# Performance work log

Hardware: AMD Instinct MI355X
Metric: run time of the kernel (lower is better)

Reference implementation:

```python
import jax, jax.numpy as jnp
import numpy as np
from itertools import product

N = 65536
G = 128          # voxel grid side
K = 27           # 3^3 kernel offsets
C_IN, C_HID, C_OUT = 3, 256, 128
EPS = 1e-5


def _build_neighbors():
    rng = np.random.default_rng(0)
    keys = np.sort(rng.choice(G ** 3, size=N, replace=False))
    coords = np.stack(np.unravel_index(keys, (G, G, G)), axis=-1)  # [N,3]
    offs = np.array(list(product([-1, 0, 1], repeat=3)), dtype=np.int64)  # [27,3]
    nc = coords[:, None, :] + offs[None, :, :]                       # [N,27,3]
    inb = ((nc >= 0) & (nc < G)).all(-1)
    nk = nc[..., 0] * G * G + nc[..., 1] * G + nc[..., 2]
    pos = np.clip(np.searchsorted(keys, np.clip(nk, 0, G ** 3 - 1)), 0, N - 1)
    found = inb & (keys[pos] == nk)
    idx = np.where(found, pos, 0).astype(np.int32)
    return idx, found


def setup_inputs() -> dict:
    key = jax.random.key(0)
    ks = jax.random.split(key, 12)
    idx, mask = _build_neighbors()
    s_in = 1.0 / np.sqrt(K * C_IN)
    s_h = 1.0 / np.sqrt(K * C_HID)
    return {
        "feats": jax.random.normal(ks[0], (N, C_IN), jnp.float32),
        "w_in": jax.random.normal(ks[1], (K, C_IN, C_HID), jnp.float32) * s_in,
        "g_in": jnp.ones((C_HID,), jnp.float32),
        "b_in": jnp.zeros((C_HID,), jnp.float32),
        "w_res": jax.random.normal(ks[2], (4, 2, K, C_HID, C_HID), jnp.float32) * s_h,
        "g_res": jnp.ones((4, 2, C_HID), jnp.float32),
        "b_res": jnp.zeros((4, 2, C_HID), jnp.float32),
        "w_out": jax.random.normal(ks[3], (C_HID, C_OUT), jnp.float32) / np.sqrt(C_HID),
        "nbr_idx": jnp.asarray(idx),
        "nbr_mask": jnp.asarray(mask),
    }


def sparse_conv(feats, W, idx, mask):
    # feats [N,Cin], W [K,Cin,Cout], idx/mask [N,K] -> gather-GEMM-scatter per offset
    def step(acc, xs):
        w_k, i_k, m_k = xs  # [Cin,Cout], [N], [N]
        g = feats[i_k] * m_k[:, None]
        return acc + g @ w_k, None
    init = jnp.zeros((feats.shape[0], W.shape[-1]), feats.dtype)
    out, _ = jax.lax.scan(step, init, (W, idx.T, mask.T.astype(feats.dtype)))
    return out


def bn(x, g, b):
    mu = x.mean(0)
    var = x.var(0)
    return (x - mu) * jax.lax.rsqrt(var + EPS) * g + b


def reference(feats, w_in, g_in, b_in, w_res, g_res, b_res, w_out, nbr_idx, nbr_mask):
    h = jax.nn.relu(bn(sparse_conv(feats, w_in, nbr_idx, nbr_mask), g_in, b_in))
    for i in range(4):  # 4 MinkowskiResBlocks
        r = jax.nn.relu(bn(sparse_conv(h, w_res[i, 0], nbr_idx, nbr_mask), g_res[i, 0], b_res[i, 0]))
        r = bn(sparse_conv(r, w_res[i, 1], nbr_idx, nbr_mask), g_res[i, 1], b_res[i, 1])
        h = jax.nn.relu(r + h)
    return h @ w_out  # kernel_size=1 output conv == pointwise linear
```

## Files before the change

### kernel.cpp

```cpp
#include <hip/hip_runtime.h>
#include <hip/hip_bf16.h>


#define NPTS 65536
#define CHID 256
#define CAP  4096
#define LBLK 256
#define CBLK 2048

typedef __bf16 bf16x8 __attribute__((ext_vector_type(8)));
typedef float  f32x4  __attribute__((ext_vector_type(4)));
typedef unsigned short u16x8 __attribute__((ext_vector_type(8)));

__device__ __forceinline__ float bf2f(unsigned short u) {
    union { float f; unsigned v; } x; x.v = ((unsigned)u) << 16; return x.f;
}
__device__ __forceinline__ unsigned short f2bf(float f) {
    union { float f; unsigned v; } x; x.f = f;
    unsigned r = x.v + 0x7fffu + ((x.v >> 16) & 1u);
    return (unsigned short)(r >> 16);
}

__device__ __forceinline__ void gload16(const void* g, void* l) {
    __builtin_amdgcn_global_load_lds(
        (const __attribute__((address_space(1))) void*)g,
        (__attribute__((address_space(3))) void*)l, 16, 0, 0);
}

__device__ __forceinline__ bool mk(const void* mask, int mflag, size_t i) {
    if (mflag) return ((const unsigned char*)mask)[i] != 0;
    return ((const int*)mask)[i] != 0;
}

__global__ void detect_mask(const unsigned char* __restrict__ m, int* __restrict__ flag) {
    int t = blockIdx.x * 256 + threadIdx.x;
    int any = 0;
    for (int i = t; i < 262144; i += 64 * 256)
        if ((i & 3) && m[i]) any = 1;
    if (any) atomicOr(flag, 1);
}

__global__ void pack_w(const float* __restrict__ w, unsigned short* __restrict__ wp) {
    __shared__ float tile[64][65];
    int m   = blockIdx.x;
    int tci = (blockIdx.y >> 2) * 64;
    int tco = (blockIdx.y & 3) * 64;
    const float* src = w + (size_t)m * 65536;
    unsigned short* dst = wp + (size_t)m * 65536;
    int t = threadIdx.x, c = t & 63, rg = t >> 6;
    for (int r = rg; r < 64; r += 4)
        tile[r][c] = src[(size_t)(tci + r) * 256 + tco + c];
    __syncthreads();
    for (int r = rg; r < 64; r += 4)
        dst[(size_t)(tco + r) * 256 + tci + c] = f2bf(tile[c][r]);
}

__global__ void pack_wout(const float* __restrict__ w, unsigned short* __restrict__ wp) {
    __shared__ float tile[64][65];
    int tco = blockIdx.x * 64, tci = blockIdx.y * 64;
    int t = threadIdx.x, c = t & 63, rg = t >> 6;
    for (int r = rg; r < 64; r += 4)
        tile[r][c] = w[(size_t)(tci + r) * 128 + tco + c];
    __syncthreads();
    for (int r = rg; r < 64; r += 4)
        wp[(size_t)(tco + r) * 256 + tci + c] = f2bf(tile[c][r]);
}

__global__ void pack_win(const float* __restrict__ w, unsigned short* __restrict__ wp) {
    __shared__ float tile[64][65];
    int cot = blockIdx.x * 64, kkt = blockIdx.y * 64;
    int t = threadIdx.x, c = t & 63, rg = t >> 6;
    for (int r = rg; r < 64; r += 4) {
        int kk = kkt + r;
        tile[r][c] = (kk < 81) ? w[(size_t)kk * 256 + cot + c] : 0.f;
    }
    __syncthreads();
    for (int r = rg; r < 64; r += 4)
        wp[(size_t)(cot + r) * 128 + kkt + c] = f2bf(tile[c][r]);
}

__global__ void count_lists(const void* __restrict__ mask, const int* __restrict__ mflagp,
                            int* __restrict__ blkcnt ) {
    int mflag = *mflagp;
    int tid = threadIdx.x, lane = tid & 63;
    int n = blockIdx.x * 256 + tid;
    __shared__ int lc[26];
    if (tid < 26) lc[tid] = 0;
    __syncthreads();
    unsigned vb = 0;
    for (int k = 0; k < 27; ++k) {
        if (k == 13) continue;
        if (mk(mask, mflag, (size_t)n * 27 + k)) vb |= 1u << k;
    }
    for (int k26 = 0; k26 < 26; ++k26) {
        int k = (k26 < 13) ? k26 : k26 + 1;
        unsigned long long b = __ballot((vb >> k) & 1);
        if (lane == 0) atomicAdd(&lc[k26], __popcll(b));
    }
    __syncthreads();
    if (tid < 26) blkcnt[tid * LBLK + blockIdx.x] = lc[tid];
}

__global__ void scan_lists(const int* __restrict__ blkcnt, int* __restrict__ bases,
                           int* __restrict__ cnt) {
    int t = threadIdx.x;
    if (t < 26) {
        int s = 0;
        for (int b = 0; b < LBLK; ++b) {
            bases[t * LBLK + b] = s;
            s += blkcnt[t * LBLK + b];
        }
        cnt[t] = s;
    }
}

__global__ void fill_lists(const int* __restrict__ idx, const void* __restrict__ mask,
                           const int* __restrict__ mflagp, const int* __restrict__ bases,
                           int* __restrict__ srcL, int* __restrict__ nbrEnt,
                           unsigned char* __restrict__ nbrCnt) {
    int mflag = *mflagp;
    int tid = threadIdx.x, lane = tid & 63, wave = tid >> 6;
    int n = blockIdx.x * 256 + tid;
    __shared__ int wcnt[4][26];
    unsigned vb = 0;
    for (int k = 0; k < 27; ++k) {
        if (k == 13) continue;
        if (mk(mask, mflag, (size_t)n * 27 + k)) vb |= 1u << k;
    }
    for (int k26 = 0; k26 < 26; ++k26) {
        int k = (k26 < 13) ? k26 : k26 + 1;
        unsigned long long b = __ballot((vb >> k) & 1);
        if (lane == 0) wcnt[wave][k26] = __popcll(b);
    }
    __syncthreads();
    int j = 0;
    for (int k26 = 0; k26 < 26; ++k26) {
        int k = (k26 < 13) ? k26 : k26 + 1;
        bool v = (vb >> k) & 1;
        unsigned long long b = __ballot(v);
        if (v) {
            int p = bases[k26 * LBLK + blockIdx.x] + __popcll(b & ((1ull << lane) - 1ull));
            for (int w = 0; w < wave; ++w) p += wcnt[w][k26];
            if (p < CAP) {
                srcL[k26 * CAP + p] = idx[(size_t)n * 27 + k];
                nbrEnt[n * 32 + j] = k26 * CAP + p;
                ++j;
            }
        }
    }
    nbrCnt[n] = (unsigned char)j;
}

__global__ __launch_bounds__(256, 2)
void convin_gemm(const float* __restrict__ feats, const unsigned short* __restrict__ win,
                 const int* __restrict__ idx, const void* __restrict__ mask,
                 const int* __restrict__ mflagp, unsigned short* __restrict__ yb) {
    __shared__ __align__(16) char A[16384];
    __shared__ __align__(16) char B[32768];
    const int mflag = *mflagp;
    const int tid = threadIdx.x, lane = tid & 63, wave = tid >> 6;
    const int m0 = blockIdx.x * 64;

    for (int i = 0; i < 4; ++i)
        *(f32x4*)&A[tid * 64 + i * 16] = f32x4{0.f, 0.f, 0.f, 0.f};
    __syncthreads();

    {
        int row = tid & 63, g = tid >> 6;
        int n = m0 + row;
        int swz = (row & 7) << 4;
        for (int k = g; k < 27; k += 4) {
            if (mk(mask, mflag, (size_t)n * 27 + k)) {
                int j = idx[(size_t)n * 27 + k];
                float f0 = feats[j * 3 + 0], f1 = feats[j * 3 + 1], f2 = feats[j * 3 + 2];
                int b0 = 2 * (3 * k + 0), b1 = b0 + 2, b2 = b0 + 4;
                *(unsigned short*)&A[row * 256 + (b0 ^ swz)] = f2bf(f0);
                *(unsigned short*)&A[row * 256 + (b1 ^ swz)] = f2bf(f1);
                *(unsigned short*)&A[row * 256 + (b2 ^ swz)] = f2bf(f2);
            }
        }
    }

    const char* wb = (const char*)win;
    f32x4 acc[4][4] = {};

    for (int ks = 0; ks < 2; ++ks) {
        __syncthreads();
        for (int i = 0; i < 8; ++i) {
            int chunk = wave * 8 + i;
            int o = chunk * 1024 + lane * 16;
            int corow = o >> 7;
            int inner = (o & 127) ^ ((corow & 7) << 4);
            gload16(wb + (size_t)corow * 256 + ks * 128 + inner, B + o);
        }
        __syncthreads();
        const int cw = wave * 64;
        for (int kk = 0; kk < 64; kk += 32) {
            int kl = kk + 8 * (lane >> 4);
            bf16x8 af[4], bfr[4];
            for (int mi = 0; mi < 4; ++mi) {
                int row = 16 * mi + (lane & 15);
                af[mi] = *(const bf16x8*)(A + row * 256 + ((ks * 128 + 2 * kl) ^ ((row & 7) << 4)));
            }
            for (int ni = 0; ni < 4; ++ni) {
                int corow = cw + 16 * ni + (lane & 15);
                bfr[ni] = *(const bf16x8*)(B + corow * 128 + ((2 * kl) ^ ((corow & 7) << 4)));
            }
            for (int mi = 0; mi < 4; ++mi)
                for (int ni = 0; ni < 4; ++ni)
                    acc[mi][ni] = __builtin_amdgcn_mfma_f32_16x16x32_bf16(af[mi], bfr[ni], acc[mi][ni], 0, 0, 0);
        }
    }

    const int cw = wave * 64;
    const int rq = 4 * (lane >> 4);
    const int colo = lane & 15;
    for (int mi = 0; mi < 4; ++mi)
        for (int ni = 0; ni < 4; ++ni) {
            int col = cw + 16 * ni + colo;
            for (int r = 0; r < 4; ++r) {
                float v = acc[mi][ni][r];
                float o = __shfl_xor(v, 1);
                if ((lane & 1) == 0) {
                    unsigned pk = (unsigned)f2bf(v) | ((unsigned)f2bf(o) << 16);
                    int row = m0 + 16 * mi + rq + r;
                    *(unsigned*)&yb[(size_t)row * CHID + col] = pk;
                }
            }
        }
}

template<bool GATHER>
__global__ __launch_bounds__(512, 1)
void conv_gemm(const unsigned short* __restrict__ hin,
               const unsigned short* __restrict__ Wp,
               unsigned short* __restrict__ yb,
               const int* __restrict__ cnt,
               const int* __restrict__ srcL) {
    __shared__ __align__(16) char lds[131072];
    __shared__ int ids_src[256];
    const int tid  = threadIdx.x;
    const int lane = tid & 63;
    const int wave = tid >> 6;
    const int wm = wave >> 2;
    const int wn = wave & 3;

    int k27 = 13, m0 = 0, k26 = 0, tile = 0, c = 0;
    if (GATHER) {
        k26 = blockIdx.x;
        k27 = (k26 < 13) ? k26 : k26 + 1;
        tile = blockIdx.y;
        c = min(cnt[k26], CAP);
        if (tile * 256 >= c) return;
        if (tid < 256) {
            int g = tile * 256 + tid;
            ids_src[tid] = (g < c) ? srcL[k26 * CAP + g] : 0;
        }
        __syncthreads();
    } else {
        m0 = blockIdx.x * 256;
    }
    const char* hbase = (const char*)hin;
    const char* wbase = (const char*)(Wp + (size_t)k27 * (CHID * CHID));

    f32x4 acc[8][4] = {};

    auto STAGE = [&](int buf, int ks) {
        const int ci0 = ks * 64;
        char* dst = lds + buf * 65536;
        #pragma unroll
        for (int i = 0; i < 8; ++i) {
            int o = (wave * 8 + i) * 1024 + lane * 16;
            const char* src;
            if (o < 32768) {
                int row = o >> 7;
                int inner = (o & 127) ^ ((row & 7) << 4);
                int grow = GATHER ? ids_src[row] : (m0 + row);
                src = hbase + (size_t)grow * 512 + ci0 * 2 + inner;
            } else {
                int bo = o - 32768;
                int corow = bo >> 7;
                int inner = (bo & 127) ^ ((corow & 7) << 4);
                src = wbase + (size_t)corow * 512 + ci0 * 2 + inner;
            }
            gload16(src, dst + o);
        }
    };

    auto COMPUTE = [&](int buf) {
        const char* A = lds + buf * 65536;
        const char* B = A + 32768;
        #pragma unroll
        for (int kk = 0; kk < 64; kk += 32) {
            int kl = kk + 8 * (lane >> 4);
            bf16x8 af[8], bfr[4];
            #pragma unroll
            for (int mi = 0; mi < 8; ++mi) {
                int row = wm * 128 + 16 * mi + (lane & 15);
                af[mi] = *(const bf16x8*)(A + row * 128 + ((2 * kl) ^ ((row & 7) << 4)));
            }
            #pragma unroll
            for (int ni = 0; ni < 4; ++ni) {
                int corow = wn * 64 + 16 * ni + (lane & 15);
                bfr[ni] = *(const bf16x8*)(B + corow * 128 + ((2 * kl) ^ ((corow & 7) << 4)));
            }
            #pragma unroll
            for (int mi = 0; mi < 8; ++mi)
                #pragma unroll
                for (int ni = 0; ni < 4; ++ni)
                    acc[mi][ni] = __builtin_amdgcn_mfma_f32_16x16x32_bf16(af[mi], bfr[ni], acc[mi][ni], 0, 0, 0);
        }
    };

    STAGE(0, 0);
    __syncthreads();
    int cur = 0;
    #pragma unroll
    for (int ks = 0; ks < 4; ++ks) {
        if (ks < 3) STAGE(cur ^ 1, ks + 1);
        COMPUTE(cur);
        __syncthreads();
        cur ^= 1;
    }

    const int rq = 4 * (lane >> 4);
    const int colo = lane & 15;
    #pragma unroll
    for (int mi = 0; mi < 8; ++mi)
        #pragma unroll
        for (int ni = 0; ni < 4; ++ni) {
            int col = wn * 64 + 16 * ni + colo;
            #pragma unroll
            for (int r = 0; r < 4; ++r) {
                float v = acc[mi][ni][r];
                float o = __shfl_xor(v, 1);
                if ((lane & 1) == 0) {
                    unsigned pk = (unsigned)f2bf(v) | ((unsigned)f2bf(o) << 16);
                    int rl = wm * 128 + 16 * mi + rq + r;
                    if (!GATHER) {
                        *(unsigned*)&yb[(size_t)(m0 + rl) * CHID + col] = pk;
                    } else {
                        int g = tile * 256 + rl;
                        if (g < c)
                            *(unsigned*)&yb[((size_t)k26 * CAP + g) * CHID + col] = pk;
                    }
                }
            }
        }
}

__global__ __launch_bounds__(256)
void combine_stats(unsigned short* __restrict__ Yb,
                   const unsigned short* __restrict__ buf,
                   const int* __restrict__ nbrEnt,
                   const unsigned char* __restrict__ nbrCnt,
                   float* __restrict__ part) {
    __shared__ float ssum[8][256];
    __shared__ float ssq[8][256];
    const int tid = threadIdx.x;
    const int grp = tid >> 5;
    const int c0  = (tid & 31) * 8;
    float s[8] = {}, s2[8] = {};
    const int row0 = blockIdx.x * 32;
    for (int it = 0; it < 4; ++it) {
        int row = row0 + it * 8 + grp;
        size_t off = (size_t)row * CHID + c0;
        u16x8 y = *(const u16x8*)&Yb[off];
        float v[8];
        #pragma unroll
        for (int q = 0; q < 8; ++q) v[q] = bf2f(y[q]);
        int cnt = nbrCnt[row];
        for (int j = 0; j < cnt; ++j) {
            int e = nbrEnt[row * 32 + j];
            u16x8 b = *(const u16x8*)&buf[(size_t)e * CHID + c0];
            #pragma unroll
            for (int q = 0; q < 8; ++q) v[q] += bf2f(b[q]);
        }
        u16x8 o;
        #pragma unroll
        for (int q = 0; q < 8; ++q) {
            o[q] = f2bf(v[q]);
            s[q] += v[q];
            s2[q] += v[q] * v[q];
        }
        *(u16x8*)&Yb[off] = o;
    }
    #pragma unroll
    for (int q = 0; q < 8; ++q) {
        ssum[grp][c0 + q] = s[q];
        ssq[grp][c0 + q]  = s2[q];
    }
    __syncthreads();
    float ts = 0.f, tq = 0.f;
    #pragma unroll
    for (int g = 0; g < 8; ++g) { ts += ssum[g][tid]; tq += ssq[g][tid]; }
    part[(size_t)blockIdx.x * 512 + tid]       = ts;
    part[(size_t)blockIdx.x * 512 + 256 + tid] = tq;
}

__global__ __launch_bounds__(256)
void bn_stats_vec(const unsigned short* __restrict__ Yb, float* __restrict__ part) {
    __shared__ float ssum[8][256];
    __shared__ float ssq[8][256];
    const int tid = threadIdx.x;
    const int grp = tid >> 5;
    const int c0  = (tid & 31) * 8;
    float s[8] = {}, s2[8] = {};
    const int row0 = blockIdx.x * 32;
    for (int it = 0; it < 4; ++it) {
        int row = row0 + it * 8 + grp;
        u16x8 y = *(const u16x8*)&Yb[(size_t)row * CHID + c0];
        #pragma unroll
        for (int q = 0; q < 8; ++q) {
            float v = bf2f(y[q]);
            s[q] += v; s2[q] += v * v;
        }
    }
    #pragma unroll
    for (int q = 0; q < 8; ++q) {
        ssum[grp][c0 + q] = s[q];
        ssq[grp][c0 + q]  = s2[q];
    }
    __syncthreads();
    float ts = 0.f, tq = 0.f;
    #pragma unroll
    for (int g = 0; g < 8; ++g) { ts += ssum[g][tid]; tq += ssq[g][tid]; }
    part[(size_t)blockIdx.x * 512 + tid]       = ts;
    part[(size_t)blockIdx.x * 512 + 256 + tid] = tq;
}

__global__ void reduce_stats(const float* __restrict__ part, float* __restrict__ st) {
    int gt = blockIdx.x * 256 + threadIdx.x;
    int c = gt & 511;
    int chunk = gt >> 9;
    float s = 0.f;
    for (int i = 0; i < CBLK / 16; ++i)
        s += part[(size_t)(chunk * (CBLK / 16) + i) * 512 + c];
    unsafeAtomicAdd(&st[c], s);
}

__global__ __launch_bounds__(256)
void bn_apply(const unsigned short* __restrict__ yb, const float* __restrict__ st,
              const float* __restrict__ g, const float* __restrict__ b,
              const unsigned short* __restrict__ res, unsigned short* __restrict__ hout) {
    const int tid = threadIdx.x;
    const int grp = tid >> 5;
    const int c0  = (tid & 31) * 8;
    float sc[8], bi[8];
    #pragma unroll
    for (int q = 0; q < 8; ++q) {
        float mean = st[c0 + q] * (1.f / NPTS);
        float var  = st[256 + c0 + q] * (1.f / NPTS) - mean * mean;
        float rstd = rsqrtf(var + 1e-5f);
        sc[q] = rstd * g[c0 + q];
        bi[q] = b[c0 + q] - mean * sc[q];
    }
    const int row0 = blockIdx.x * 32;
    for (int it = 0; it < 4; ++it) {
        int row = row0 + it * 8 + grp;
        size_t off = (size_t)row * CHID + c0;
        u16x8 y = *(const u16x8*)&yb[off];
        u16x8 o;
        if (res) {
            u16x8 rr = *(const u16x8*)&res[off];
            #pragma unroll
            for (int q = 0; q < 8; ++q) {
                float v = bf2f(y[q]) * sc[q] + bi[q] + bf2f(rr[q]);
                o[q] = f2bf(fmaxf(v, 0.f));
            }
        } else {
            #pragma unroll
            for (int q = 0; q < 8; ++q) {
                float v = bf2f(y[q]) * sc[q] + bi[q];
                o[q] = f2bf(fmaxf(v, 0.f));
            }
        }
        *(u16x8*)&hout[off] = o;
    }
}

__global__ __launch_bounds__(256, 2)
void gemm_out(const unsigned short* __restrict__ hin, const unsigned short* __restrict__ wop,
              float* __restrict__ out) {
    __shared__ __align__(16) char lds[16384 + 16384];
    const int tid = threadIdx.x, lane = tid & 63, wave = tid >> 6;
    const int m0 = blockIdx.x * 128;
    const char* hb = (const char*)hin;
    const char* wb = (const char*)wop;
    f32x4 acc[4][4] = {};
    for (int ks = 0; ks < 4; ++ks) {
        int ci0 = ks * 64;
        __syncthreads();
        for (int i = 0; i < 8; ++i) {
            int chunk = wave * 8 + i;
            int o = chunk * 1024 + lane * 16;
            const char* src;
            if (o < 16384) {
                int row = o >> 7;
                int k2 = (o & 127) ^ ((row & 7) << 4);
                src = hb + (size_t)(m0 + row) * 512 + ci0 * 2 + k2;
            } else {
                int bo = o - 16384;
                int corow = bo >> 7;
                int k2 = (bo & 127) ^ ((corow & 7) << 4);
                src = wb + (size_t)corow * 512 + ci0 * 2 + k2;
            }
            gload16(src, lds + chunk * 1024);
        }
        __syncthreads();
        const char* A = lds;
        const char* B = lds + 16384;
        const int wm = wave >> 1, wn = wave & 1;
        for (int kk = 0; kk < 64; kk += 32) {
            int kl = kk + 8 * (lane >> 4);
            bf16x8 af[4], bfr[4];
            for (int mi = 0; mi < 4; ++mi) {
                int row = 64 * wm + 16 * mi + (lane & 15);
                af[mi] = *(const bf16x8*)(A + row * 128 + ((2 * kl) ^ ((row & 7) << 4)));
            }
            for (int ni = 0; ni < 4; ++ni) {
                int corow = 64 * wn + 16 * ni + (lane & 15);
                bfr[ni] = *(const bf16x8*)(B + corow * 128 + ((2 * kl) ^ ((corow & 7) << 4)));
            }
            for (int mi = 0; mi < 4; ++mi)
                for (int ni = 0; ni < 4; ++ni)
                    acc[mi][ni] = __builtin_amdgcn_mfma_f32_16x16x32_bf16(af[mi], bfr[ni], acc[mi][ni], 0, 0, 0);
        }
    }
    const int wm = wave >> 1, wn = wave & 1;
    for (int mi = 0; mi < 4; ++mi)
        for (int ni = 0; ni < 4; ++ni) {
            int col = 64 * wn + 16 * ni + (lane & 15);
            for (int r = 0; r < 4; ++r) {
                int row = m0 + 64 * wm + 16 * mi + 4 * (lane >> 4) + r;
                out[(size_t)row * 128 + col] = acc[mi][ni][r];
            }
        }
}

static const size_t OFF_Y    = 0;
static const size_t OFF_HA   = OFF_Y   + (size_t)NPTS * CHID * 2;
static const size_t OFF_HR   = OFF_HA  + (size_t)NPTS * CHID * 2;
static const size_t OFF_WP   = OFF_HR  + (size_t)NPTS * CHID * 2;
static const size_t OFF_WOP  = OFF_WP  + (size_t)8 * 27 * 65536 * 2;
static const size_t OFF_WIN  = OFF_WOP + (size_t)128 * 256 * 2;
static const size_t OFF_ST   = OFF_WIN + (size_t)256 * 128 * 2;
static const size_t OFF_CNT  = OFF_ST  + 9 * 512 * 4;
static const size_t OFF_FLAG = OFF_CNT + 112;
static const size_t OFF_SRC  = OFF_CNT + 128;
static const size_t OFF_BLK  = OFF_SRC + (size_t)26 * CAP * 4;
static const size_t OFF_BAS  = OFF_BLK + (size_t)26 * LBLK * 4;
static const size_t OFF_NBE  = OFF_BAS + (size_t)26 * LBLK * 4;
static const size_t OFF_NBC  = OFF_NBE + (size_t)NPTS * 32 * 4;
static const size_t OFF_PART = OFF_NBC + (size_t)NPTS;
static const size_t OFF_BUF  = OFF_PART + (size_t)CBLK * 512 * 4;

extern "C" void kernel_launch(void* const* d_in, const int* in_sizes, int n_in,
                              void* d_out, int out_size, void* d_ws, size_t ws_size,
                              hipStream_t stream) {
    const float* feats = (const float*)d_in[0];
    const float* w_in  = (const float*)d_in[1];
    const float* g_in  = (const float*)d_in[2];
    const float* b_in  = (const float*)d_in[3];
    const float* w_res = (const float*)d_in[4];
    const float* g_res = (const float*)d_in[5];
    const float* b_res = (const float*)d_in[6];
    const float* w_out = (const float*)d_in[7];
    const int*   nidx  = (const int*)d_in[8];
    const void*  nmask = (const void*)d_in[9];

    char* ws = (char*)d_ws;
    unsigned short* Yb   = (unsigned short*)(ws + OFF_Y);
    unsigned short* HA   = (unsigned short*)(ws + OFF_HA);
    unsigned short* HR   = (unsigned short*)(ws + OFF_HR);
    unsigned short* WP   = (unsigned short*)(ws + OFF_WP);
    unsigned short* WOP  = (unsigned short*)(ws + OFF_WOP);
    unsigned short* WIN  = (unsigned short*)(ws + OFF_WIN);
    float*          ST   = (float*)(ws + OFF_ST);
    int*            CNT  = (int*)(ws + OFF_CNT);
    int*            MFLG = (int*)(ws + OFF_FLAG);
    int*            SRCL = (int*)(ws + OFF_SRC);
    int*            BLKC = (int*)(ws + OFF_BLK);
    int*            BASE = (int*)(ws + OFF_BAS);
    int*            NBE  = (int*)(ws + OFF_NBE);
    unsigned char*  NBC  = (unsigned char*)(ws + OFF_NBC);
    float*          PART = (float*)(ws + OFF_PART);
    unsigned short* BUF  = (unsigned short*)(ws + OFF_BUF);

    hipMemsetAsync(ws + OFF_ST, 0, 9 * 512 * 4 + 128, stream);

    detect_mask<<<64, 256, 0, stream>>>((const unsigned char*)nmask, MFLG);
    pack_w   <<<dim3(216, 16), 256, 0, stream>>>(w_res, WP);
    pack_wout<<<dim3(2, 4),    256, 0, stream>>>(w_out, WOP);
    pack_win <<<dim3(4, 2),    256, 0, stream>>>(w_in, WIN);

    count_lists<<<LBLK, 256, 0, stream>>>(nmask, MFLG, BLKC);
    scan_lists <<<1, 64, 0, stream>>>(BLKC, BASE, CNT);
    fill_lists <<<LBLK, 256, 0, stream>>>(nidx, nmask, MFLG, BASE, SRCL, NBE, NBC);

    convin_gemm<<<NPTS / 64, 256, 0, stream>>>(feats, WIN, nidx, nmask, MFLG, Yb);
    bn_stats_vec<<<CBLK, 256, 0, stream>>>(Yb, PART);
    reduce_stats<<<32, 256, 0, stream>>>(PART, ST);
    bn_apply<<<CBLK, 256, 0, stream>>>(Yb, ST, g_in, b_in, nullptr, HA);

    for (int c8 = 0; c8 < 8; ++c8) {
        const unsigned short* hin = (c8 & 1) ? HR : HA;
        const unsigned short* wbase = WP + (size_t)c8 * 27 * 65536;
        float* st = ST + (size_t)(1 + c8) * 512;
        conv_gemm<false><<<NPTS / 256, 512, 0, stream>>>(hin, wbase, Yb, nullptr, nullptr);
        conv_gemm<true><<<dim3(26, CAP / 256), 512, 0, stream>>>(hin, wbase, BUF, CNT, SRCL);
        combine_stats<<<CBLK, 256, 0, stream>>>(Yb, BUF, NBE, NBC, PART);
        reduce_stats<<<32, 256, 0, stream>>>(PART, st);
        if (c8 & 1) {
            bn_apply<<<CBLK, 256, 0, stream>>>(Yb, st, g_res + c8 * 256, b_res + c8 * 256, HA, HA);
        } else {
            bn_apply<<<CBLK, 256, 0, stream>>>(Yb, st, g_res + c8 * 256, b_res + c8 * 256, nullptr, HR);
        }
    }

    gemm_out<<<NPTS / 128, 256, 0, stream>>>(HA, WOP, (float*)d_out);
}
```

Before: 788.0 us.

## Merge dense and gather conv GEMMs into one launch; fuse input-conv BN stats

The dense center-offset GEMM and the per-offset gather GEMMs are combined into a single kernel launch, with block index deciding the role. This removes one launch per conv and lets the two sets of blocks run concurrently, filling the GPU better. The input conv's epilogue also computes per-block column sums and squared sums, replacing the separate bn_stats pass over Yb. reduce_stats now takes the block count as a parameter.

```diff
diff --git a/kernel.cpp b/kernel.cpp
--- a/kernel.cpp
+++ b/kernel.cpp
@@ -154,9 +154,11 @@
 __global__ __launch_bounds__(256, 2)
 void convin_gemm(const float* __restrict__ feats, const unsigned short* __restrict__ win,
                  const int* __restrict__ idx, const void* __restrict__ mask,
-                 const int* __restrict__ mflagp, unsigned short* __restrict__ yb) {
+                 const int* __restrict__ mflagp, unsigned short* __restrict__ yb,
+                 float* __restrict__ part) {
     __shared__ __align__(16) char A[16384];
     __shared__ __align__(16) char B[32768];
+    __shared__ float psum[512];
     const int mflag = *mflagp;
     const int tid = threadIdx.x, lane = tid & 63, wave = tid >> 6;
     const int m0 = blockIdx.x * 64;
@@ -215,11 +217,13 @@
     const int cw = wave * 64;
     const int rq = 4 * (lane >> 4);
     const int colo = lane & 15;
+    float cs[4] = {}, cq[4] = {};
     for (int mi = 0; mi < 4; ++mi)
         for (int ni = 0; ni < 4; ++ni) {
             int col = cw + 16 * ni + colo;
             for (int r = 0; r < 4; ++r) {
                 float v = acc[mi][ni][r];
+                cs[ni] += v; cq[ni] += v * v;
                 float o = __shfl_xor(v, 1);
                 if ((lane & 1) == 0) {
                     unsigned pk = (unsigned)f2bf(v) | ((unsigned)f2bf(o) << 16);
@@ -228,15 +232,30 @@
                 }
             }
         }
-}
-
-template<bool GATHER>
+    #pragma unroll
+    for (int ni = 0; ni < 4; ++ni) {
+        float s = cs[ni], q = cq[ni];
+        s += __shfl_down(s, 32); q += __shfl_down(q, 32);
+        s += __shfl_down(s, 16); q += __shfl_down(q, 16);
+        if (lane < 16) {
+            psum[cw + 16 * ni + lane]       = s;
+            psum[256 + cw + 16 * ni + lane] = q;
+        }
+    }
+    __syncthreads();
+    if (tid < 256) {
+        part[(size_t)blockIdx.x * 512 + tid]       = psum[tid];
+        part[(size_t)blockIdx.x * 512 + 256 + tid] = psum[256 + tid];
+    }
+}
+
 __global__ __launch_bounds__(512, 1)
-void conv_gemm(const unsigned short* __restrict__ hin,
-               const unsigned short* __restrict__ Wp,
-               unsigned short* __restrict__ yb,
-               const int* __restrict__ cnt,
-               const int* __restrict__ srcL) {
+void conv_fused(const unsigned short* __restrict__ hin,
+                const unsigned short* __restrict__ Wp,
+                unsigned short* __restrict__ yb,
+                unsigned short* __restrict__ bufo,
+                const int* __restrict__ cnt,
+                const int* __restrict__ srcL) {
     __shared__ __align__(16) char lds[131072];
     __shared__ int ids_src[256];
     const int tid  = threadIdx.x;
@@ -245,21 +264,24 @@
     const int wm = wave >> 2;
     const int wn = wave & 3;
 
+    const bool GAT = blockIdx.x >= (NPTS / 256);
     int k27 = 13, m0 = 0, k26 = 0, tile = 0, c = 0;
-    if (GATHER) {
-        k26 = blockIdx.x;
+    if (GAT) {
+        int e = blockIdx.x - (NPTS / 256);
+        k26 = e >> 4;
+        tile = e & 15;
         k27 = (k26 < 13) ? k26 : k26 + 1;
-        tile = blockIdx.y;
         c = min(cnt[k26], CAP);
         if (tile * 256 >= c) return;
         if (tid < 256) {
             int g = tile * 256 + tid;
             ids_src[tid] = (g < c) ? srcL[k26 * CAP + g] : 0;
         }
-        __syncthreads();
     } else {
         m0 = blockIdx.x * 256;
     }
+    __syncthreads();
+
     const char* hbase = (const char*)hin;
     const char* wbase = (const char*)(Wp + (size_t)k27 * (CHID * CHID));
 
@@ -275,7 +297,7 @@
             if (o < 32768) {
                 int row = o >> 7;
                 int inner = (o & 127) ^ ((row & 7) << 4);
-                int grow = GATHER ? ids_src[row] : (m0 + row);
+                int grow = GAT ? ids_src[row] : (m0 + row);
                 src = hbase + (size_t)grow * 512 + ci0 * 2 + inner;
             } else {
                 int bo = o - 32768;
@@ -337,12 +359,12 @@
                 if ((lane & 1) == 0) {
                     unsigned pk = (unsigned)f2bf(v) | ((unsigned)f2bf(o) << 16);
                     int rl = wm * 128 + 16 * mi + rq + r;
-                    if (!GATHER) {
+                    if (!GAT) {
                         *(unsigned*)&yb[(size_t)(m0 + rl) * CHID + col] = pk;
                     } else {
                         int g = tile * 256 + rl;
                         if (g < c)
-                            *(unsigned*)&yb[((size_t)k26 * CAP + g) * CHID + col] = pk;
+                            *(unsigned*)&bufo[((size_t)k26 * CAP + g) * CHID + col] = pk;
                     }
                 }
             }
@@ -398,44 +420,15 @@
     part[(size_t)blockIdx.x * 512 + 256 + tid] = tq;
 }
 
-__global__ __launch_bounds__(256)
-void bn_stats_vec(const unsigned short* __restrict__ Yb, float* __restrict__ part) {
-    __shared__ float ssum[8][256];
-    __shared__ float ssq[8][256];
-    const int tid = threadIdx.x;
-    const int grp = tid >> 5;
-    const int c0  = (tid & 31) * 8;
-    float s[8] = {}, s2[8] = {};
-    const int row0 = blockIdx.x * 32;
-    for (int it = 0; it < 4; ++it) {
-        int row = row0 + it * 8 + grp;
-        u16x8 y = *(const u16x8*)&Yb[(size_t)row * CHID + c0];
-        #pragma unroll
-        for (int q = 0; q < 8; ++q) {
-            float v = bf2f(y[q]);
-            s[q] += v; s2[q] += v * v;
-        }
-    }
-    #pragma unroll
-    for (int q = 0; q < 8; ++q) {
-        ssum[grp][c0 + q] = s[q];
-        ssq[grp][c0 + q]  = s2[q];
-    }
-    __syncthreads();
-    float ts = 0.f, tq = 0.f;
-    #pragma unroll
-    for (int g = 0; g < 8; ++g) { ts += ssum[g][tid]; tq += ssq[g][tid]; }
-    part[(size_t)blockIdx.x * 512 + tid]       = ts;
-    part[(size_t)blockIdx.x * 512 + 256 + tid] = tq;
-}
-
-__global__ void reduce_stats(const float* __restrict__ part, float* __restrict__ st) {
+__global__ void reduce_stats(const float* __restrict__ part, float* __restrict__ st,
+                             int nblk) {
     int gt = blockIdx.x * 256 + threadIdx.x;
     int c = gt & 511;
     int chunk = gt >> 9;
+    int per = nblk / 16;
     float s = 0.f;
-    for (int i = 0; i < CBLK / 16; ++i)
-        s += part[(size_t)(chunk * (CBLK / 16) + i) * 512 + c];
+    for (int i = 0; i < per; ++i)
+        s += part[(size_t)(chunk * per + i) * 512 + c];
     unsafeAtomicAdd(&st[c], s);
 }
 
@@ -598,19 +591,18 @@
     scan_lists <<<1, 64, 0, stream>>>(BLKC, BASE, CNT);
     fill_lists <<<LBLK, 256, 0, stream>>>(nidx, nmask, MFLG, BASE, SRCL, NBE, NBC);
 
-    convin_gemm<<<NPTS / 64, 256, 0, stream>>>(feats, WIN, nidx, nmask, MFLG, Yb);
-    bn_stats_vec<<<CBLK, 256, 0, stream>>>(Yb, PART);
-    reduce_stats<<<32, 256, 0, stream>>>(PART, ST);
+    convin_gemm<<<NPTS / 64, 256, 0, stream>>>(feats, WIN, nidx, nmask, MFLG, Yb, PART);
+    reduce_stats<<<32, 256, 0, stream>>>(PART, ST, NPTS / 64);
     bn_apply<<<CBLK, 256, 0, stream>>>(Yb, ST, g_in, b_in, nullptr, HA);
 
+    const int GRID_CONV = NPTS / 256 + 26 * (CAP / 256);
     for (int c8 = 0; c8 < 8; ++c8) {
         const unsigned short* hin = (c8 & 1) ? HR : HA;
         const unsigned short* wbase = WP + (size_t)c8 * 27 * 65536;
         float* st = ST + (size_t)(1 + c8) * 512;
-        conv_gemm<false><<<NPTS / 256, 512, 0, stream>>>(hin, wbase, Yb, nullptr, nullptr);
-        conv_gemm<true><<<dim3(26, CAP / 256), 512, 0, stream>>>(hin, wbase, BUF, CNT, SRCL);
+        conv_fused<<<GRID_CONV, 512, 0, stream>>>(hin, wbase, Yb, BUF, CNT, SRCL);
         combine_stats<<<CBLK, 256, 0, stream>>>(Yb, BUF, NBE, NBC, PART);
-        reduce_stats<<<32, 256, 0, stream>>>(PART, st);
+        reduce_stats<<<32, 256, 0, stream>>>(PART, st, CBLK);
         if (c8 & 1) {
             bn_apply<<<CBLK, 256, 0, stream>>>(Yb, st, g_res + c8 * 256, b_res + c8 * 256, HA, HA);
         } else {
```

Result: slower. 1.172 ms (+48.7%).
